# Performance work log

Hardware: AMD Instinct MI355X
Metric: run time of the kernel (lower is better)

The kernel has to match this reference:

```python
import jax, jax.numpy as jnp
import numpy as np

N, D = 1024, 8192

def setup_inputs() -> dict:
    key = jax.random.key(0)
    k1, k2 = jax.random.split(key)
    pred = jax.random.normal(k1, (N, D), dtype=jnp.float32)
    eeg = jax.random.normal(k2, (N, D), dtype=jnp.float32)
    return {"pred": pred, "eeg": eeg}

def _ranks(x):
    # rank transform along last axis (no ties expected for continuous data):
    # argsort of argsort gives 0-based ranks, matching spearman rank order.
    order = jnp.argsort(x, axis=-1)
    return jnp.argsort(order, axis=-1).astype(x.dtype)

def _normed_ranks(x):
    r = _ranks(x)  # [n, D]
    r = r - jnp.mean(r, axis=-1, keepdims=True)
    return r / jnp.linalg.norm(r, axis=-1, keepdims=True)

def reference(pred, eeg):
    # base criterion: MSELoss (as used in the repo)
    loss1 = jnp.mean((pred - eeg) ** 2)
    # all-pairs spearman correlation via one batched rank + single GEMM,
    # replacing the original O(n^2) python loop of tiny ops.
    rp = _normed_ranks(pred)   # [n, D]
    re_ = _normed_ranks(eeg)   # [n, D]
    corr = rp @ re_.T          # [n, n] pairwise spearman coefficients
    n = pred.shape[0]
    pos = jnp.mean(jnp.diagonal(corr))
    off_mask = ~jnp.eye(n, dtype=bool)
    neg = jnp.sum(jnp.where(off_mask, corr, 0.0)) / (n * (n - 1))
    # original builds loss2 from torch.tensor(list) -> detached from autograd
    loss2 = jax.lax.stop_gradient(1.0 - pos + neg)
    return loss1 + loss2
```

## Files before the change

### kernel.cpp

```cpp
#include <hip/hip_runtime.h>
#include <stdint.h>

#define NROW 1024
#define DCOL 8192
#define T1   1024
#define EPT  8

typedef unsigned long long u64;

__device__ __forceinline__ uint32_t sortable_key(float f){
  uint32_t u = __float_as_uint(f);
  return u ^ ((uint32_t)((int32_t)u >> 31) | 0x80000000u);
}

extern "C" __global__ void __launch_bounds__(T1)
rank_kernel(const float* __restrict__ pred, const float* __restrict__ eeg,
            uint16_t* __restrict__ ranks, double* __restrict__ msepart)
{
  __shared__ uint32_t h[DCOL];
  __shared__ uint32_t g[DCOL];
  __shared__ uint32_t wt[16];
  __shared__ double   redd[16];

  const int t = threadIdx.x;
  const int pair = blockIdx.x >> 1;
  const bool is_eeg = blockIdx.x & 1;
  const int lane = t & 63, wid = t >> 6;
  const float* src = is_eeg ? (eeg  + (size_t)pair * DCOL)
                            : (pred + (size_t)pair * DCOL);

  const float4* s4 = (const float4*)(src + t * EPT);
  float4 va = s4[0], vb = s4[1];

  {
    uint4 z = make_uint4(0u,0u,0u,0u);
    *(uint4*)&h[t*EPT]   = z;
    *(uint4*)&h[t*EPT+4] = z;
    *(uint4*)&g[t*EPT]   = z;
    *(uint4*)&g[t*EPT+4] = z;
  }

  double msum = 0.0;
  if (is_eeg){
    const float4* p4 = (const float4*)(pred + (size_t)pair * DCOL + t * EPT);
    float4 qa = p4[0], qb = p4[1];
    float d;
    d=qa.x-va.x; msum += (double)(d*d);
    d=qa.y-va.y; msum += (double)(d*d);
    d=qa.z-va.z; msum += (double)(d*d);
    d=qa.w-va.w; msum += (double)(d*d);
    d=qb.x-vb.x; msum += (double)(d*d);
    d=qb.y-vb.y; msum += (double)(d*d);
    d=qb.z-vb.z; msum += (double)(d*d);
    d=qb.w-vb.w; msum += (double)(d*d);
  }

  uint32_t key[EPT];
  key[0]=sortable_key(va.x); key[1]=sortable_key(va.y);
  key[2]=sortable_key(va.z); key[3]=sortable_key(va.w);
  key[4]=sortable_key(vb.x); key[5]=sortable_key(vb.y);
  key[6]=sortable_key(vb.z); key[7]=sortable_key(vb.w);
  __syncthreads();

  #pragma unroll
  for (int j=0;j<EPT;j++) atomicAdd(&h[key[j]>>19], 1u);
  __syncthreads();

  {
    uint4 ca = *(const uint4*)&h[t*EPT];
    uint4 cb = *(const uint4*)&h[t*EPT+4];
    uint32_t tot = ca.x+ca.y+ca.z+ca.w+cb.x+cb.y+cb.z+cb.w;
    uint32_t v = tot;
    #pragma unroll
    for (int o=1;o<64;o<<=1){ uint32_t u=__shfl_up(v,o,64); if(lane>=o) v+=u; }
    if (lane==63) wt[wid]=v;
    __syncthreads();
    uint32_t run = v - tot;
    #pragma unroll
    for (int w=0;w<16;w++) run += (w<wid)? wt[w] : 0u;
    uint4 oa, ob;
    oa.x=(run<<16)|ca.x; run+=ca.x;
    oa.y=(run<<16)|ca.y; run+=ca.y;
    oa.z=(run<<16)|ca.z; run+=ca.z;
    oa.w=(run<<16)|ca.w; run+=ca.w;
    ob.x=(run<<16)|cb.x; run+=cb.x;
    ob.y=(run<<16)|cb.y; run+=cb.y;
    ob.z=(run<<16)|cb.z; run+=cb.z;
    ob.w=(run<<16)|cb.w; run+=cb.w;
    *(uint4*)&h[t*EPT]   = oa;
    *(uint4*)&h[t*EPT+4] = ob;
  }
  __syncthreads();

  uint32_t b2[EPT], e[EPT];
  #pragma unroll
  for (int j=0;j<EPT;j++){
    uint32_t hi = key[j]>>19, lo = key[j]&0x7FFFFu;
    uint32_t v  = h[hi];
    b2[j] = (v>>16) + ((lo*(v&0xFFFFu))>>19);
    e[j]  = (lo<<13) | (uint32_t)(t*EPT+j);
    atomicAdd(&g[b2[j]], 1u);
  }
  __syncthreads();

  {
    uint4 ca = *(const uint4*)&g[t*EPT];
    uint4 cb = *(const uint4*)&g[t*EPT+4];
    uint32_t tot = ca.x+ca.y+ca.z+ca.w+cb.x+cb.y+cb.z+cb.w;
    uint32_t v = tot;
    #pragma unroll
    for (int o=1;o<64;o<<=1){ uint32_t u=__shfl_up(v,o,64); if(lane>=o) v+=u; }
    if (lane==63) wt[wid]=v;
    __syncthreads();
    uint32_t run = v - tot;
    #pragma unroll
    for (int w=0;w<16;w++) run += (w<wid)? wt[w] : 0u;
    uint4 oa, ob;
    oa.x=(run<<16)|run; run+=ca.x;
    oa.y=(run<<16)|run; run+=ca.y;
    oa.z=(run<<16)|run; run+=ca.z;
    oa.w=(run<<16)|run; run+=ca.w;
    ob.x=(run<<16)|run; run+=cb.x;
    ob.y=(run<<16)|run; run+=cb.y;
    ob.z=(run<<16)|run; run+=cb.z;
    ob.w=(run<<16)|run; run+=cb.w;
    *(uint4*)&g[t*EPT]   = oa;
    *(uint4*)&g[t*EPT+4] = ob;
  }
  __syncthreads();

  uint32_t old[EPT];
  #pragma unroll
  for (int j=0;j<EPT;j++){
    old[j] = atomicAdd(&g[b2[j]], 1u);
    h[old[j] & 0xFFFFu] = e[j];
  }
  __syncthreads();

  uint32_t rk[EPT];
  #pragma unroll
  for (int j=0;j<EPT;j++){
    uint32_t st = old[j] >> 16;
    uint32_t en = g[b2[j]] & 0xFFFFu;
    uint32_t cnt = 0;
    for (uint32_t p = st; p < en; ++p) cnt += (h[p] < e[j]) ? 1u : 0u;
    rk[j] = st + cnt;
  }

  uint4 pk;
  pk.x = rk[0] | (rk[1]<<16);
  pk.y = rk[2] | (rk[3]<<16);
  pk.z = rk[4] | (rk[5]<<16);
  pk.w = rk[6] | (rk[7]<<16);
  const size_t orow = is_eeg ? (size_t)(NROW + pair) : (size_t)pair;
  *(uint4*)(ranks + orow*DCOL + (size_t)t*EPT) = pk;

  if (is_eeg){
    #pragma unroll
    for (int o=32;o>0;o>>=1) msum += __shfl_down(msum,o,64);
    if (lane==0) redd[wid]=msum;
    __syncthreads();
    if (t==0){
      double m=0.0;
      #pragma unroll
      for (int w=0;w<16;w++) m += redd[w];
      msepart[pair]=m;
    }
  }
}

extern "C" __global__ void __launch_bounds__(256)
colsum_part_kernel(const uint16_t* __restrict__ ranks,
                   u64* __restrict__ SABpart, u64* __restrict__ dotpart)
{
  __shared__ u64 redu[4];
  const int t = threadIdx.x;
  const int bx = blockIdx.x, by = blockIdx.y;
  const int col = bx*2048 + t*8;
  const int r0  = by*16;
  const uint16_t* rp = ranks;
  const uint16_t* re = ranks + (size_t)NROW*DCOL;
  uint32_t sa[8] = {0,0,0,0,0,0,0,0};
  uint32_t sb[8] = {0,0,0,0,0,0,0,0};
  u64 dt = 0ull;
  #pragma unroll
  for (int i=0;i<16;i++){
    uint4 a = *(const uint4*)&rp[(size_t)(r0+i)*DCOL + col];
    uint4 b = *(const uint4*)&re[(size_t)(r0+i)*DCOL + col];
    uint32_t aw[8] = {a.x&0xFFFFu,a.x>>16,a.y&0xFFFFu,a.y>>16,
                      a.z&0xFFFFu,a.z>>16,a.w&0xFFFFu,a.w>>16};
    uint32_t bw[8] = {b.x&0xFFFFu,b.x>>16,b.y&0xFFFFu,b.y>>16,
                      b.z&0xFFFFu,b.z>>16,b.w&0xFFFFu,b.w>>16};
    uint32_t rowdt = 0;
    #pragma unroll
    for (int k=0;k<8;k++){ sa[k]+=aw[k]; sb[k]+=bw[k]; rowdt += aw[k]*bw[k]; }
    dt += (u64)rowdt;
  }
  u64* dst = SABpart + (size_t)by*DCOL + col;
  #pragma unroll
  for (int k=0;k<8;k++) dst[k] = (u64)sa[k] | ((u64)sb[k]<<32);

  #pragma unroll
  for (int o=32;o>0;o>>=1) dt += __shfl_down(dt,o,64);
  int lane=t&63, wid=t>>6;
  if (lane==0) redu[wid]=dt;
  __syncthreads();
  if (t==0) dotpart[by*4+bx] = redu[0]+redu[1]+redu[2]+redu[3];
}

extern "C" __global__ void __launch_bounds__(128)
reduce_kernel(const u64* __restrict__ SABpart, u64* __restrict__ SAB)
{
  const int col = blockIdx.x*128 + threadIdx.x;
  u64 s = 0ull;
  #pragma unroll
  for (int by=0; by<64; by++) s += SABpart[(size_t)by*DCOL + col];
  SAB[col] = s;
}

extern "C" __global__ void __launch_bounds__(256)
final_part_kernel(const u64* __restrict__ SAB, const u64* __restrict__ dotpart,
                  const double* __restrict__ msepart, float* __restrict__ out)
{
  __shared__ double wpartd[4], wpartm[4];
  __shared__ u64 wpartu[4];
  const int t = threadIdx.x;
  const double NMU = 4193792.0;
  double s = 0.0;
  for (int i=0;i<DCOL/256;i++){
    u64 v = SAB[i*256+t];
    s += ((double)(uint32_t)v - NMU)*((double)(uint32_t)(v>>32) - NMU);
  }
  double m = 0.0;
  for (int i=t;i<NROW;i+=256) m += msepart[i];
  u64 d = dotpart[t];
  #pragma unroll
  for (int o=32;o>0;o>>=1){
    s+=__shfl_down(s,o,64); m+=__shfl_down(m,o,64); d+=__shfl_down(d,o,64);
  }
  int lane=t&63, wid=t>>6;
  if (lane==0){ wpartd[wid]=s; wpartm[wid]=m; wpartu[wid]=d; }
  __syncthreads();
  if (t==0){
    double sasb   = wpartd[0]+wpartd[1]+wpartd[2]+wpartd[3];
    double msesum = wpartm[0]+wpartm[1]+wpartm[2]+wpartm[3];
    double dot    = (double)(wpartu[0]+wpartu[1]+wpartu[2]+wpartu[3]);
    const double C     = 45812983808.0;
    const double NDMU2 = 140703130714112.0;
    double diag_sum = (dot - NDMU2) / C;
    double pos = diag_sum / (double)NROW;
    double stotal = sasb / C;
    double neg = (stotal - diag_sum) / ((double)NROW*(double)(NROW-1));
    double loss1 = msesum / ((double)NROW*(double)DCOL);
    out[0] = (float)(loss1 + 1.0 - pos + neg);
  }
}

extern "C" __global__ void __launch_bounds__(256)
colsum_atomic_kernel(const uint16_t* __restrict__ ranks,
                     u64* __restrict__ SAB, u64* __restrict__ dotacc)
{
  const int t = threadIdx.x;
  const int col = blockIdx.x*2048 + t*8;
  const int r0  = blockIdx.y*16;
  const uint16_t* rp = ranks;
  const uint16_t* re = ranks + (size_t)NROW*DCOL;
  uint32_t sa[8] = {0,0,0,0,0,0,0,0};
  uint32_t sb[8] = {0,0,0,0,0,0,0,0};
  u64 dt = 0ull;
  for (int i=0;i<16;i++){
    uint4 a = *(const uint4*)&rp[(size_t)(r0+i)*DCOL + col];
    uint4 b = *(const uint4*)&re[(size_t)(r0+i)*DCOL + col];
    uint32_t aw[8] = {a.x&0xFFFFu,a.x>>16,a.y&0xFFFFu,a.y>>16,
                      a.z&0xFFFFu,a.z>>16,a.w&0xFFFFu,a.w>>16};
    uint32_t bw[8] = {b.x&0xFFFFu,b.x>>16,b.y&0xFFFFu,b.y>>16,
                      b.z&0xFFFFu,b.z>>16,b.w&0xFFFFu,b.w>>16};
    uint32_t rowdt = 0;
    #pragma unroll
    for (int k=0;k<8;k++){ sa[k]+=aw[k]; sb[k]+=bw[k]; rowdt += aw[k]*bw[k]; }
    dt += (u64)rowdt;
  }
  #pragma unroll
  for (int k=0;k<8;k++)
    atomicAdd(&SAB[col+k], (u64)sa[k] | ((u64)sb[k]<<32));
  #pragma unroll
  for (int o=32;o>0;o>>=1) dt += __shfl_down(dt,o,64);
  if ((t&63)==0) atomicAdd(dotacc, dt);
}

extern "C" __global__ void __launch_bounds__(256)
final_atomic_kernel(const u64* __restrict__ SAB, const u64* __restrict__ dotacc,
                    const double* __restrict__ msepart, float* __restrict__ out)
{
  __shared__ double wpartd[4], wpartm[4];
  const int t = threadIdx.x;
  const double NMU = 4193792.0;
  double s = 0.0;
  for (int i=0;i<DCOL/256;i++){
    u64 v = SAB[i*256+t];
    s += ((double)(uint32_t)v - NMU)*((double)(uint32_t)(v>>32) - NMU);
  }
  double m = 0.0;
  for (int i=t;i<NROW;i+=256) m += msepart[i];
  #pragma unroll
  for (int o=32;o>0;o>>=1){ s+=__shfl_down(s,o,64); m+=__shfl_down(m,o,64); }
  int lane=t&63, wid=t>>6;
  if (lane==0){ wpartd[wid]=s; wpartm[wid]=m; }
  __syncthreads();
  if (t==0){
    double sasb   = wpartd[0]+wpartd[1]+wpartd[2]+wpartd[3];
    double msesum = wpartm[0]+wpartm[1]+wpartm[2]+wpartm[3];
    const double C     = 45812983808.0;
    const double NDMU2 = 140703130714112.0;
    double dot = (double)(*dotacc);
    double diag_sum = (dot - NDMU2) / C;
    double pos = diag_sum / (double)NROW;
    double stotal = sasb / C;
    double neg = (stotal - diag_sum) / ((double)NROW*(double)(NROW-1));
    double loss1 = msesum / ((double)NROW*(double)DCOL);
    out[0] = (float)(loss1 + 1.0 - pos + neg);
  }
}

extern "C" void kernel_launch(void* const* d_in, const int* in_sizes, int n_in,
                              void* d_out, int out_size, void* d_ws, size_t ws_size,
                              hipStream_t stream)
{
  const float* pred = (const float*)d_in[0];
  const float* eeg  = (const float*)d_in[1];
  float* out = (float*)d_out;

  char* ws = (char*)d_ws;
  const size_t OFF       = (size_t)2*NROW*DCOL*sizeof(uint16_t);
  const size_t SZ_PART   = (size_t)64*DCOL*sizeof(u64);
  const size_t NEED_PART = OFF + SZ_PART + DCOL*sizeof(u64) + 256*sizeof(u64)
                           + NROW*sizeof(double);
  const size_t NEED_ATOM = OFF + DCOL*sizeof(u64) + 8 + NROW*sizeof(double);

  if (ws_size >= NEED_PART){
    uint16_t* ranks  = (uint16_t*)ws;
    u64* SABpart     = (u64*)(ws + OFF);
    u64* SAB         = (u64*)(ws + OFF + SZ_PART);
    u64* dotpart     = (u64*)(ws + OFF + SZ_PART + DCOL*sizeof(u64));
    double* msepart  = (double*)(ws + OFF + SZ_PART + DCOL*sizeof(u64) + 256*sizeof(u64));

    rank_kernel<<<dim3(2*NROW), dim3(T1), 0, stream>>>(pred, eeg, ranks, msepart);
    colsum_part_kernel<<<dim3(4,64), dim3(256), 0, stream>>>(ranks, SABpart, dotpart);
    reduce_kernel<<<dim3(64), dim3(128), 0, stream>>>(SABpart, SAB);
    final_part_kernel<<<dim3(1), dim3(256), 0, stream>>>(SAB, dotpart, msepart, out);
  } else if (ws_size >= NEED_ATOM){
    uint16_t* ranks  = (uint16_t*)ws;
    u64* SAB         = (u64*)(ws + OFF);
    u64* dotacc      = (u64*)(ws + OFF + DCOL*sizeof(u64));
    double* msepart  = (double*)(ws + OFF + DCOL*sizeof(u64) + 8);

    hipMemsetAsync(ws + OFF, 0, DCOL*sizeof(u64) + 8, stream);
    rank_kernel<<<dim3(2*NROW), dim3(T1), 0, stream>>>(pred, eeg, ranks, msepart);
    colsum_atomic_kernel<<<dim3(4,64), dim3(256), 0, stream>>>(ranks, SAB, dotacc);
    final_atomic_kernel<<<dim3(1), dim3(256), 0, stream>>>(SAB, dotacc, msepart, out);
  } else {
    hipMemsetAsync(d_out, 0xFF, sizeof(float), stream);
  }
}
```

Before: 79.37 us.

## Tweak rank kernel scans, block mapping, and fold column products into reduce

Remaps rank-kernel blocks so groups of eight pred rows and eight eeg rows alternate, changing the scheduling and memory locality pattern. Replaces the serial 16-iteration warp-total prefix with a shuffle reduction, uses a 24-bit multiply, and skips the within-bucket comparison loop for singleton buckets. The colsum kernel moves to smaller 128-thread blocks over more columns. The centered column-sum product is computed in the reduce kernel, so the final single-block kernel only sums 64 partials. These are small independent tweaks aimed at shaving latency in the dominant rank kernel and the serial final step.

```diff
diff --git a/kernel.cpp b/kernel.cpp
--- a/kernel.cpp
+++ b/kernel.cpp
@@ -23,8 +23,9 @@
   __shared__ double   redd[16];
 
   const int t = threadIdx.x;
-  const int pair = blockIdx.x >> 1;
-  const bool is_eeg = blockIdx.x & 1;
+  const int bid = blockIdx.x;
+  const int pair = ((bid >> 4) << 3) | (bid & 7);
+  const bool is_eeg = (bid >> 3) & 1;
   const int lane = t & 63, wid = t >> 6;
   const float* src = is_eeg ? (eeg  + (size_t)pair * DCOL)
                             : (pred + (size_t)pair * DCOL);
@@ -75,9 +76,10 @@
     for (int o=1;o<64;o<<=1){ uint32_t u=__shfl_up(v,o,64); if(lane>=o) v+=u; }
     if (lane==63) wt[wid]=v;
     __syncthreads();
-    uint32_t run = v - tot;
-    #pragma unroll
-    for (int w=0;w<16;w++) run += (w<wid)? wt[w] : 0u;
+    uint32_t x = (lane < wid) ? wt[lane] : 0u;
+    #pragma unroll
+    for (int o=32;o>0;o>>=1) x += __shfl_xor(x, o, 64);
+    uint32_t run = x + v - tot;
     uint4 oa, ob;
     oa.x=(run<<16)|ca.x; run+=ca.x;
     oa.y=(run<<16)|ca.y; run+=ca.y;
@@ -97,7 +99,7 @@
   for (int j=0;j<EPT;j++){
     uint32_t hi = key[j]>>19, lo = key[j]&0x7FFFFu;
     uint32_t v  = h[hi];
-    b2[j] = (v>>16) + ((lo*(v&0xFFFFu))>>19);
+    b2[j] = (v>>16) + (__umul24(lo, v&0xFFFFu)>>19);
     e[j]  = (lo<<13) | (uint32_t)(t*EPT+j);
     atomicAdd(&g[b2[j]], 1u);
   }
@@ -112,9 +114,10 @@
     for (int o=1;o<64;o<<=1){ uint32_t u=__shfl_up(v,o,64); if(lane>=o) v+=u; }
     if (lane==63) wt[wid]=v;
     __syncthreads();
-    uint32_t run = v - tot;
-    #pragma unroll
-    for (int w=0;w<16;w++) run += (w<wid)? wt[w] : 0u;
+    uint32_t x = (lane < wid) ? wt[lane] : 0u;
+    #pragma unroll
+    for (int o=32;o>0;o>>=1) x += __shfl_xor(x, o, 64);
+    uint32_t run = x + v - tot;
     uint4 oa, ob;
     oa.x=(run<<16)|run; run+=ca.x;
     oa.y=(run<<16)|run; run+=ca.y;
@@ -143,7 +146,9 @@
     uint32_t st = old[j] >> 16;
     uint32_t en = g[b2[j]] & 0xFFFFu;
     uint32_t cnt = 0;
-    for (uint32_t p = st; p < en; ++p) cnt += (h[p] < e[j]) ? 1u : 0u;
+    if (en - st > 1){
+      for (uint32_t p = st; p < en; ++p) cnt += (h[p] < e[j]) ? 1u : 0u;
+    }
     rk[j] = st + cnt;
   }
 
@@ -169,14 +174,14 @@
   }
 }
 
-extern "C" __global__ void __launch_bounds__(256)
+extern "C" __global__ void __launch_bounds__(128)
 colsum_part_kernel(const uint16_t* __restrict__ ranks,
                    u64* __restrict__ SABpart, u64* __restrict__ dotpart)
 {
-  __shared__ u64 redu[4];
+  __shared__ u64 redu[2];
   const int t = threadIdx.x;
   const int bx = blockIdx.x, by = blockIdx.y;
-  const int col = bx*2048 + t*8;
+  const int col = bx*1024 + t*8;
   const int r0  = by*16;
   const uint16_t* rp = ranks;
   const uint16_t* re = ranks + (size_t)NROW*DCOL;
@@ -205,35 +210,39 @@
   int lane=t&63, wid=t>>6;
   if (lane==0) redu[wid]=dt;
   __syncthreads();
-  if (t==0) dotpart[by*4+bx] = redu[0]+redu[1]+redu[2]+redu[3];
+  if (t==0) dotpart[by*8+bx] = redu[0]+redu[1];
 }
 
 extern "C" __global__ void __launch_bounds__(128)
-reduce_kernel(const u64* __restrict__ SABpart, u64* __restrict__ SAB)
-{
-  const int col = blockIdx.x*128 + threadIdx.x;
+reduce2_kernel(const u64* __restrict__ SABpart, double* __restrict__ Spart)
+{
+  __shared__ double red[2];
+  const int t = threadIdx.x;
+  const int col = blockIdx.x*128 + t;
   u64 s = 0ull;
   #pragma unroll
   for (int by=0; by<64; by++) s += SABpart[(size_t)by*DCOL + col];
-  SAB[col] = s;
+  const double NMU = 4193792.0;
+  double d = ((double)(uint32_t)s - NMU) * ((double)(uint32_t)(s>>32) - NMU);
+  #pragma unroll
+  for (int o=32;o>0;o>>=1) d += __shfl_down(d,o,64);
+  int lane=t&63, wid=t>>6;
+  if (lane==0) red[wid]=d;
+  __syncthreads();
+  if (t==0) Spart[blockIdx.x] = red[0]+red[1];
 }
 
 extern "C" __global__ void __launch_bounds__(256)
-final_part_kernel(const u64* __restrict__ SAB, const u64* __restrict__ dotpart,
-                  const double* __restrict__ msepart, float* __restrict__ out)
+final_kernel(const double* __restrict__ Spart, const u64* __restrict__ dotpart,
+             const double* __restrict__ msepart, float* __restrict__ out)
 {
   __shared__ double wpartd[4], wpartm[4];
   __shared__ u64 wpartu[4];
   const int t = threadIdx.x;
-  const double NMU = 4193792.0;
-  double s = 0.0;
-  for (int i=0;i<DCOL/256;i++){
-    u64 v = SAB[i*256+t];
-    s += ((double)(uint32_t)v - NMU)*((double)(uint32_t)(v>>32) - NMU);
-  }
+  double s = (t < 64) ? Spart[t] : 0.0;
+  u64 d = dotpart[t] + dotpart[t+256];
   double m = 0.0;
   for (int i=t;i<NROW;i+=256) m += msepart[i];
-  u64 d = dotpart[t];
   #pragma unroll
   for (int o=32;o>0;o>>=1){
     s+=__shfl_down(s,o,64); m+=__shfl_down(m,o,64); d+=__shfl_down(d,o,64);
@@ -333,21 +342,21 @@
   char* ws = (char*)d_ws;
   const size_t OFF       = (size_t)2*NROW*DCOL*sizeof(uint16_t);
   const size_t SZ_PART   = (size_t)64*DCOL*sizeof(u64);
-  const size_t NEED_PART = OFF + SZ_PART + DCOL*sizeof(u64) + 256*sizeof(u64)
+  const size_t NEED_PART = OFF + SZ_PART + 64*sizeof(double) + 512*sizeof(u64)
                            + NROW*sizeof(double);
   const size_t NEED_ATOM = OFF + DCOL*sizeof(u64) + 8 + NROW*sizeof(double);
 
   if (ws_size >= NEED_PART){
     uint16_t* ranks  = (uint16_t*)ws;
     u64* SABpart     = (u64*)(ws + OFF);
-    u64* SAB         = (u64*)(ws + OFF + SZ_PART);
-    u64* dotpart     = (u64*)(ws + OFF + SZ_PART + DCOL*sizeof(u64));
-    double* msepart  = (double*)(ws + OFF + SZ_PART + DCOL*sizeof(u64) + 256*sizeof(u64));
+    double* Spart    = (double*)(ws + OFF + SZ_PART);
+    u64* dotpart     = (u64*)(ws + OFF + SZ_PART + 64*sizeof(double));
+    double* msepart  = (double*)(ws + OFF + SZ_PART + 64*sizeof(double) + 512*sizeof(u64));
 
     rank_kernel<<<dim3(2*NROW), dim3(T1), 0, stream>>>(pred, eeg, ranks, msepart);
-    colsum_part_kernel<<<dim3(4,64), dim3(256), 0, stream>>>(ranks, SABpart, dotpart);
-    reduce_kernel<<<dim3(64), dim3(128), 0, stream>>>(SABpart, SAB);
-    final_part_kernel<<<dim3(1), dim3(256), 0, stream>>>(SAB, dotpart, msepart, out);
+    colsum_part_kernel<<<dim3(8,64), dim3(128), 0, stream>>>(ranks, SABpart, dotpart);
+    reduce2_kernel<<<dim3(64), dim3(128), 0, stream>>>(SABpart, Spart);
+    final_kernel<<<dim3(1), dim3(256), 0, stream>>>(Spart, dotpart, msepart, out);
   } else if (ws_size >= NEED_ATOM){
     uint16_t* ranks  = (uint16_t*)ws;
     u64* SAB         = (u64*)(ws + OFF);
```

New measurement: 77.65 us. 2.2% less time.
